# Kernel tuning notes

Hardware: AMD Instinct MI355X
Metric: run time of the kernel (lower is better)

Reference implementation:

```python
import jax, jax.numpy as jnp
import numpy as np

B, C, H, W = 4, 64, 128, 128
KH, KW = 5, 5
PAD = 2
HEADS, DIM_HEAD = 8, 8


def setup_inputs() -> dict:
    key = jax.random.key(0)
    k1, k2, k3, k4 = jax.random.split(key, 4)
    return {
        "features1": jax.random.normal(k1, (B, C, H, W), dtype=jnp.float32),
        "features2": jax.random.normal(k2, (B, C, H, W), dtype=jnp.float32),
        "rel_h": jax.random.normal(k3, (C // 2, 1, 1, KH, 1), dtype=jnp.float32),
        "rel_w": jax.random.normal(k4, (C // 2, 1, 1, 1, KW), dtype=jnp.float32),
    }


def reference(features1, features2, rel_h, rel_w):
    b, c, h, w = features1.shape
    K = KH * KW
    # pad key/value source spatially
    padded = jnp.pad(features2, ((0, 0), (0, 0), (PAD, PAD), (PAD, PAD)))
    # materialize sliding windows: [B, C, H, W, KH*KW], kw index minor (matches torch unfold(2).unfold(3))
    windows = jnp.stack(
        [padded[:, :, i:i + h, j:j + w] for i in range(KH) for j in range(KW)],
        axis=-1,
    )
    # relative position bias: first C/2 channels get rel_h, last C/2 get rel_w
    relh = jnp.broadcast_to(rel_h.reshape(c // 2, KH, 1), (c // 2, KH, KW))
    relw = jnp.broadcast_to(rel_w.reshape(c // 2, 1, KW), (c // 2, KH, KW))
    rel = jnp.concatenate([relh, relw], axis=0).reshape(c, K)  # [C, K]
    k = windows + rel[None, :, None, None, :]
    v = windows
    q = features1.reshape(b, HEADS, DIM_HEAD, h, w, 1)
    k = k.reshape(b, HEADS, DIM_HEAD, h, w, K)
    v = v.reshape(b, HEADS, DIM_HEAD, h, w, K)
    # per-channel windowed softmax attention (no reduction over channel in scores)
    attn = jax.nn.softmax(q * k, axis=-1)
    # einsum 'abcdef,abcdef->acbde' from torch: output is [B, dim_head, heads, H, W]
    out = jnp.einsum('bhcxyk,bhcxyk->bchxy', attn, v)
    return out.reshape(b, c, h, w)
```

## Files before the change

### kernel.cpp

```cpp
#include <hip/hip_runtime.h>

#define B_ 4
#define C_ 64
#define H_ 128
#define W_ 128
#define R_ 8
#define LOG2E 1.44269504088896340736f

template<int HALF>
__device__ __forceinline__ void sa_body(int x, int y0,
    const float* __restrict__ f1p, const float* __restrict__ f2p,
    const float* __restrict__ relp, float* __restrict__ outp)
{
    float rel5[5];
    #pragma unroll
    for (int k = 0; k < 5; ++k) rel5[k] = relp[k];

    int coff[5]; float msk[5];
    #pragma unroll
    for (int j = 0; j < 5; ++j) {
        const int kx = x + j - 2;
        coff[j] = kx < 0 ? 0 : (kx > W_ - 1 ? W_ - 1 : kx);
        msk[j]  = (kx >= 0 && kx < W_) ? 1.0f : 0.0f;
    }

    float win[5][5];
    #pragma unroll
    for (int t = 0; t < 4; ++t) {
        const int ky = y0 + t - 2;
        if (ky >= 0) {
            const float* rp = f2p + ky * W_;
            #pragma unroll
            for (int j = 0; j < 5; ++j) win[t][j] = rp[coff[j]] * msk[j];
        } else {
            #pragma unroll
            for (int j = 0; j < 5; ++j) win[t][j] = 0.0f;
        }
    }

    #pragma unroll
    for (int r = 0; r < R_; ++r) {
        {
            const int ky = y0 + r + 2;
            const int slot = (r + 4) % 5;
            if (ky < H_) {
                const float* rp = f2p + ky * W_;
                #pragma unroll
                for (int j = 0; j < 5; ++j) win[slot][j] = rp[coff[j]] * msk[j];
            } else {
                #pragma unroll
                for (int j = 0; j < 5; ++j) win[slot][j] = 0.0f;
            }
        }

        const int y = y0 + r;
        const float q2 = f1p[y * W_ + x] * LOG2E;
        float prel[5];
        #pragma unroll
        for (int k = 0; k < 5; ++k) prel[k] = q2 * rel5[k];

        float sum0 = 0.f, sum1 = 0.f, dot0 = 0.f, dot1 = 0.f;
        #pragma unroll
        for (int i = 0; i < 5; ++i) {
            #pragma unroll
            for (int j = 0; j < 5; ++j) {
                const float v  = win[(r + i) % 5][j];
                const float sc = __builtin_fmaf(q2, v, prel[HALF == 0 ? i : j]);
                const float p  = __builtin_amdgcn_exp2f(sc);
                if (((i * 5 + j) & 1) == 0) { sum0 += p; dot0 = __builtin_fmaf(p, v, dot0); }
                else                        { sum1 += p; dot1 = __builtin_fmaf(p, v, dot1); }
            }
        }
        outp[y * W_ + x] = __fdividef(dot0 + dot1, sum0 + sum1);
    }
}

__global__ __launch_bounds__(256) void sa_kernel(
    const float* __restrict__ f1, const float* __restrict__ f2,
    const float* __restrict__ relh, const float* __restrict__ relw,
    float* __restrict__ out)
{
    const int tid   = threadIdx.x;
    const int x     = tid & (W_ - 1);
    const int s     = tid >> 7;
    const int blk   = blockIdx.x;
    const int spair = blk & 7;
    const int bc    = blk >> 3;
    const int c     = bc & (C_ - 1);
    const int b     = bc >> 6;
    const int y0    = __builtin_amdgcn_readfirstlane((spair * 2 + s) * R_);

    const size_t img = (size_t)(b * C_ + c) * (H_ * W_);
    const float* f1p = f1 + img;
    const float* f2p = f2 + img;

    const int c_out = (c & 7) * 8 + (c >> 3);
    float* outp = out + (size_t)(b * C_ + c_out) * (H_ * W_);

    if (c < C_ / 2) sa_body<0>(x, y0, f1p, f2p, relh + c * 5, outp);
    else            sa_body<1>(x, y0, f1p, f2p, relw + (c - C_ / 2) * 5, outp);
}

extern "C" void kernel_launch(void* const* d_in, const int* in_sizes, int n_in,
                              void* d_out, int out_size, void* d_ws, size_t ws_size,
                              hipStream_t stream) {
    const float* f1   = (const float*)d_in[0];
    const float* f2   = (const float*)d_in[1];
    const float* relh = (const float*)d_in[2];
    const float* relw = (const float*)d_in[3];
    float* out = (float*)d_out;

    const int grid = B_ * C_ * (H_ / R_ / 2);
    sa_kernel<<<grid, 256, 0, stream>>>(f1, f2, relh, relw, out);
}
```

Baseline: 26.84 us.

## Replace hardware exp2 with packed-FP32 polynomial exp2 and vectorize softmax math

Swaps the transcendental v_exp_f32 for a software exp2: round-to-nearest via a magic-constant add, a cubic polynomial for the fraction, and exponent insertion by integer shift-add. The window, score, sum and dot arithmetic is regrouped into float2 vectors so the compiler can emit packed FP32 ops (v_pk_fma/v_pk_add). The aim is to move exp work off the quarter-rate transcendental unit onto full-rate packed ALUs. In exchange it costs extra instructions per exp and loses accuracy: the cubic is only approximate, and there is no overflow or underflow handling for large-magnitude scores.

```diff
diff --git a/kernel.cpp b/kernel.cpp
--- a/kernel.cpp
+++ b/kernel.cpp
@@ -7,14 +7,39 @@
 #define R_ 8
 #define LOG2E 1.44269504088896340736f
 
+typedef float        v2f __attribute__((ext_vector_type(2)));
+typedef unsigned int v2u __attribute__((ext_vector_type(2)));
+
+__device__ __forceinline__ v2f exp2p2(v2f x) {
+    v2f t  = x + 12582912.0f;
+    v2f nf = t - 12582912.0f;
+    v2f f  = x - nf;
+    v2f p  = __builtin_elementwise_fma((v2f){0.0555041086f, 0.0555041086f}, f,
+                                       (v2f){0.2402265070f, 0.2402265070f});
+    p = __builtin_elementwise_fma(p, f, (v2f){0.6931471806f, 0.6931471806f});
+    p = __builtin_elementwise_fma(p, f, (v2f){1.0f, 1.0f});
+    v2u e = __builtin_bit_cast(v2u, t) << 23;
+    return __builtin_bit_cast(v2f, __builtin_bit_cast(v2u, p) + e);
+}
+__device__ __forceinline__ float exp2p1(float x) {
+    float t  = x + 12582912.0f;
+    float nf = t - 12582912.0f;
+    float f  = x - nf;
+    float p  = __builtin_fmaf(0.0555041086f, f, 0.2402265070f);
+    p = __builtin_fmaf(p, f, 0.6931471806f);
+    p = __builtin_fmaf(p, f, 1.0f);
+    unsigned e = __builtin_bit_cast(unsigned, t) << 23;
+    return __builtin_bit_cast(float, __builtin_bit_cast(unsigned, p) + e);
+}
+
 template<int HALF>
 __device__ __forceinline__ void sa_body(int x, int y0,
     const float* __restrict__ f1p, const float* __restrict__ f2p,
     const float* __restrict__ relp, float* __restrict__ outp)
 {
-    float rel5[5];
-    #pragma unroll
-    for (int k = 0; k < 5; ++k) rel5[k] = relp[k];
+    v2f   rl01 = {relp[0], relp[1]};
+    v2f   rl23 = {relp[2], relp[3]};
+    float rl4  = relp[4];
 
     int coff[5]; float msk[5];
     #pragma unroll
@@ -24,17 +49,18 @@
         msk[j]  = (kx >= 0 && kx < W_) ? 1.0f : 0.0f;
     }
 
-    float win[5][5];
+    v2f wa[5], wb[5]; float wc[5];
+
     #pragma unroll
     for (int t = 0; t < 4; ++t) {
         const int ky = y0 + t - 2;
         if (ky >= 0) {
             const float* rp = f2p + ky * W_;
-            #pragma unroll
-            for (int j = 0; j < 5; ++j) win[t][j] = rp[coff[j]] * msk[j];
+            wa[t] = (v2f){ rp[coff[0]] * msk[0], rp[coff[1]] * msk[1] };
+            wb[t] = (v2f){ rp[coff[2]],          rp[coff[3]] * msk[3] };
+            wc[t] = rp[coff[4]] * msk[4];
         } else {
-            #pragma unroll
-            for (int j = 0; j < 5; ++j) win[t][j] = 0.0f;
+            wa[t] = (v2f){0.f, 0.f}; wb[t] = (v2f){0.f, 0.f}; wc[t] = 0.f;
         }
     }
 
@@ -45,33 +71,60 @@
             const int slot = (r + 4) % 5;
             if (ky < H_) {
                 const float* rp = f2p + ky * W_;
-                #pragma unroll
-                for (int j = 0; j < 5; ++j) win[slot][j] = rp[coff[j]] * msk[j];
+                wa[slot] = (v2f){ rp[coff[0]] * msk[0], rp[coff[1]] * msk[1] };
+                wb[slot] = (v2f){ rp[coff[2]],          rp[coff[3]] * msk[3] };
+                wc[slot] = rp[coff[4]] * msk[4];
             } else {
-                #pragma unroll
-                for (int j = 0; j < 5; ++j) win[slot][j] = 0.0f;
+                wa[slot] = (v2f){0.f, 0.f}; wb[slot] = (v2f){0.f, 0.f}; wc[slot] = 0.f;
             }
         }
 
         const int y = y0 + r;
         const float q2 = f1p[y * W_ + x] * LOG2E;
-        float prel[5];
-        #pragma unroll
-        for (int k = 0; k < 5; ++k) prel[k] = q2 * rel5[k];
+        const v2f q2v = {q2, q2};
+        const v2f prA = q2v * rl01;
+        const v2f prB = q2v * rl23;
+        const float prC = q2 * rl4;
 
-        float sum0 = 0.f, sum1 = 0.f, dot0 = 0.f, dot1 = 0.f;
+        v2f sA = {0.f, 0.f}, dA = {0.f, 0.f};
+        v2f sB = {0.f, 0.f}, dB = {0.f, 0.f};
+        float ss = 0.f, ds = 0.f;
+
         #pragma unroll
         for (int i = 0; i < 5; ++i) {
-            #pragma unroll
-            for (int j = 0; j < 5; ++j) {
-                const float v  = win[(r + i) % 5][j];
-                const float sc = __builtin_fmaf(q2, v, prel[HALF == 0 ? i : j]);
-                const float p  = __builtin_amdgcn_exp2f(sc);
-                if (((i * 5 + j) & 1) == 0) { sum0 += p; dot0 = __builtin_fmaf(p, v, dot0); }
-                else                        { sum1 += p; dot1 = __builtin_fmaf(p, v, dot1); }
-            }
+            const int sl = (r + i) % 5;
+            const float pri = (i == 0) ? prA.x : (i == 1) ? prA.y
+                            : (i == 2) ? prB.x : (i == 3) ? prB.y : prC;
+            const v2f pra = (HALF == 0) ? (v2f){pri, pri} : prA;
+            const v2f prb = (HALF == 0) ? (v2f){pri, pri} : prB;
+            {   const v2f v = wa[sl];
+                const v2f sc = __builtin_elementwise_fma(v, q2v, pra);
+                const v2f p  = exp2p2(sc);
+                sA += p; dA = __builtin_elementwise_fma(p, v, dA); }
+            {   const v2f v = wb[sl];
+                const v2f sc = __builtin_elementwise_fma(v, q2v, prb);
+                const v2f p  = exp2p2(sc);
+                sB += p; dB = __builtin_elementwise_fma(p, v, dB); }
         }
-        outp[y * W_ + x] = __fdividef(dot0 + dot1, sum0 + sum1);
+        {   const v2f v  = { wc[(r + 0) % 5], wc[(r + 1) % 5] };
+            const v2f pr = (HALF == 0) ? prA : (v2f){prC, prC};
+            const v2f sc = __builtin_elementwise_fma(v, q2v, pr);
+            const v2f p  = exp2p2(sc);
+            sA += p; dA = __builtin_elementwise_fma(p, v, dA); }
+        {   const v2f v  = { wc[(r + 2) % 5], wc[(r + 3) % 5] };
+            const v2f pr = (HALF == 0) ? prB : (v2f){prC, prC};
+            const v2f sc = __builtin_elementwise_fma(v, q2v, pr);
+            const v2f p  = exp2p2(sc);
+            sB += p; dB = __builtin_elementwise_fma(p, v, dB); }
+        {   const float v  = wc[(r + 4) % 5];
+            const float sc = __builtin_fmaf(q2, v, prC);
+            const float p  = exp2p1(sc);
+            ss += p; ds = __builtin_fmaf(p, v, ds); }
+
+        const v2f st = sA + sB, dt = dA + dB;
+        const float sum = st.x + st.y + ss;
+        const float dot = dt.x + dt.y + ds;
+        outp[y * W_ + x] = __fdividef(dot, sum);
     }
 }
 
```

New measurement: 34.12 us. 27.1% more time.

## Halve rows per thread and preload the whole window before computing

Applied to the files above, without the earlier changes.

Cuts rows per thread from 8 to 4, which doubles the grid, and loads all 8 window rows plus the q values up front instead of streaming one row per iteration through a rotating buffer. Issuing every load first is meant to expose more memory-level parallelism and raise occupancy. The division is also replaced with a hardware reciprocal. In exchange, each thread re-reads more halo rows relative to the outputs it produces (8 input rows for 4 output rows, instead of 12 for 8), and the preloaded window uses more registers.

```diff
diff --git a/kernel.cpp b/kernel.cpp
--- a/kernel.cpp
+++ b/kernel.cpp
@@ -4,7 +4,8 @@
 #define C_ 64
 #define H_ 128
 #define W_ 128
-#define R_ 8
+#define R_ 4
+#define NROWS (R_ + 4)
 #define LOG2E 1.44269504088896340736f
 
 template<int HALF>
@@ -24,37 +25,32 @@
         msk[j]  = (kx >= 0 && kx < W_) ? 1.0f : 0.0f;
     }
 
-    float win[5][5];
+    float w[NROWS][5];
     #pragma unroll
-    for (int t = 0; t < 4; ++t) {
+    for (int t = 0; t < NROWS; ++t) {
         const int ky = y0 + t - 2;
-        if (ky >= 0) {
+        if (ky >= 0 && ky < H_) {
             const float* rp = f2p + ky * W_;
             #pragma unroll
-            for (int j = 0; j < 5; ++j) win[t][j] = rp[coff[j]] * msk[j];
+            for (int j = 0; j < 5; ++j) w[t][j] = rp[coff[j]];
         } else {
             #pragma unroll
-            for (int j = 0; j < 5; ++j) win[t][j] = 0.0f;
+            for (int j = 0; j < 5; ++j) w[t][j] = 0.0f;
         }
+    }
+    float qv[R_];
+    #pragma unroll
+    for (int r = 0; r < R_; ++r) qv[r] = f1p[(y0 + r) * W_ + x];
+
+    #pragma unroll
+    for (int t = 0; t < NROWS; ++t) {
+        #pragma unroll
+        for (int j = 0; j < 5; ++j) w[t][j] *= msk[j];
     }
 
     #pragma unroll
     for (int r = 0; r < R_; ++r) {
-        {
-            const int ky = y0 + r + 2;
-            const int slot = (r + 4) % 5;
-            if (ky < H_) {
-                const float* rp = f2p + ky * W_;
-                #pragma unroll
-                for (int j = 0; j < 5; ++j) win[slot][j] = rp[coff[j]] * msk[j];
-            } else {
-                #pragma unroll
-                for (int j = 0; j < 5; ++j) win[slot][j] = 0.0f;
-            }
-        }
-
-        const int y = y0 + r;
-        const float q2 = f1p[y * W_ + x] * LOG2E;
+        const float q2 = qv[r] * LOG2E;
         float prel[5];
         #pragma unroll
         for (int k = 0; k < 5; ++k) prel[k] = q2 * rel5[k];
@@ -64,14 +60,16 @@
         for (int i = 0; i < 5; ++i) {
             #pragma unroll
             for (int j = 0; j < 5; ++j) {
-                const float v  = win[(r + i) % 5][j];
+                const float v  = w[r + i][j];
                 const float sc = __builtin_fmaf(q2, v, prel[HALF == 0 ? i : j]);
                 const float p  = __builtin_amdgcn_exp2f(sc);
                 if (((i * 5 + j) & 1) == 0) { sum0 += p; dot0 = __builtin_fmaf(p, v, dot0); }
                 else                        { sum1 += p; dot1 = __builtin_fmaf(p, v, dot1); }
             }
         }
-        outp[y * W_ + x] = __fdividef(dot0 + dot1, sum0 + sum1);
+        const float sum = sum0 + sum1;
+        const float dot = dot0 + dot1;
+        outp[(y0 + r) * W_ + x] = dot * __builtin_amdgcn_rcpf(sum);
     }
 }
 
@@ -84,8 +82,8 @@
     const int x     = tid & (W_ - 1);
     const int s     = tid >> 7;
     const int blk   = blockIdx.x;
-    const int spair = blk & 7;
-    const int bc    = blk >> 3;
+    const int spair = blk & (H_ / R_ / 2 - 1);
+    const int bc    = blk >> 4;
     const int c     = bc & (C_ - 1);
     const int b     = bc >> 6;
     const int y0    = __builtin_amdgcn_readfirstlane((spair * 2 + s) * R_);
```

New measurement: 24.93 us. 1.08x faster.
